# Kernel optimization log

Hardware: AMD Instinct MI355X
Metric: run time of the kernel (lower is better)

The kernel has to match this reference:

```python
import jax, jax.numpy as jnp
import numpy as np

B, T, F, U = 64, 256, 64, 512  # batch, bid_sequence, features, lstm units


def setup_inputs() -> dict:
    key = jax.random.key(0)
    ks = jax.random.split(key, 8)
    sc = 0.05
    return {
        "inputs": jax.random.normal(ks[0], (B, T, F), jnp.float32),
        "kernel": jax.random.normal(ks[1], (F, 4 * U), jnp.float32) * sc,      # LSTM input kernel (i,f,c,o)
        "rec_kernel": jax.random.normal(ks[2], (U, 4 * U), jnp.float32) * sc,  # LSTM recurrent kernel
        "bias": jax.random.normal(ks[3], (4 * U,), jnp.float32) * sc,          # LSTM bias
        "att_W": jax.random.normal(ks[4], (T, T), jnp.float32) * sc,           # row t = weights of attention_denses[t] (first t cols used)
        "att_b": jax.random.normal(ks[5], (T,), jnp.float32) * sc,             # bias of attention_denses[t]
        "out_W": jax.random.normal(ks[6], (U,), jnp.float32) * sc,             # final Dense(1) kernel
        "out_b": jax.random.normal(ks[7], (), jnp.float32) * sc,               # final Dense(1) bias
    }


def reference(inputs, kernel, rec_kernel, bias, att_W, att_b, out_W, out_b):
    Bs, Ts, _ = inputs.shape
    Us = rec_kernel.shape[0]

    # ---- LSTM (keras LSTMCell, gate order i,f,c,o; sigmoid/tanh) ----
    xz = jnp.einsum('btf,fg->btg', inputs, kernel) + bias  # precompute input projection

    def step(carry, z):
        h, c = carry
        g = z + h @ rec_kernel
        i, f, gc, o = jnp.split(g, 4, axis=-1)
        c = jax.nn.sigmoid(f) * c + jax.nn.sigmoid(i) * jnp.tanh(gc)
        h = jax.nn.sigmoid(o) * jnp.tanh(c)
        return (h, c), h

    init = (jnp.zeros((Bs, Us), inputs.dtype), jnp.zeros((Bs, Us), inputs.dtype))
    _, hs = jax.lax.scan(step, init, jnp.swapaxes(xz, 0, 1))
    x = jnp.swapaxes(hs, 0, 1)  # (B, T, U)

    # ---- attention_loop ----
    # keras Attention([x[:t], [x[t]]]) softmaxes over a single key -> weights are
    # exactly 1, so attn output is x[t] tiled t times; transpose + Dense_t(1)
    # collapses to sum(att_W[t, :t]) * x[t] + att_b[t]. Step 0 passes x[0] through.
    t_idx = jnp.arange(Ts)
    tri = (t_idx[None, :] < t_idx[:, None]).astype(x.dtype)  # row t: first t cols valid
    coef = jnp.where(t_idx == 0, jnp.asarray(1.0, x.dtype), jnp.sum(att_W * tri, axis=1))
    shift = jnp.where(t_idx == 0, jnp.asarray(0.0, x.dtype), att_b)
    att = x * coef[None, :, None] + shift[None, :, None]  # (B, T, U)

    # ---- final Dense(1) + reshape + sigmoid ----
    return jax.nn.sigmoid(jnp.einsum('btu,u->bt', att, out_W) + out_b)  # (B, T)
```

## Files before the change

kernel.cpp:

```cpp
#include <hip/hip_runtime.h>
#include <hip/hip_bf16.h>
#include <string.h>

#define B_ 64
#define T_ 256
#define F_ 64
#define U_ 512
#define G4_ 2048
#define KTOT 576
#define KSTEPS 18

typedef __attribute__((ext_vector_type(8))) short short8;
typedef __attribute__((ext_vector_type(4))) float v4f;
typedef __attribute__((ext_vector_type(4))) int i4;
typedef unsigned short u16;

__device__ __forceinline__ float bf2f(u16 b) {
    unsigned int x = ((unsigned int)b) << 16;
    float f; memcpy(&f, &x, 4); return f;
}
__device__ __forceinline__ u16 f2bf(float f) {
    __hip_bfloat16 h = __float2bfloat16(f);
    u16 b; memcpy(&b, &h, 2); return b;
}
__device__ __forceinline__ float sigmoidf_(float x) { return 1.f / (1.f + __expf(-x)); }
__device__ __forceinline__ float tanhf_(float x) {
    float xc = fminf(15.f, fmaxf(-15.f, x));
    float e = __expf(2.f * xc);
    return (e - 1.f) / (e + 1.f);
}

__device__ __forceinline__ float ldany(const void* p, size_t i, int fg) {
    return fg ? ((const float*)p)[i] : bf2f(((const u16*)p)[i]);
}

#define WS_FLAG   0
#define WS_XB     64
#define WS_WP     2097216
#define WS_H2     4456512
#define WS_DOT    4718656
#define WS_BIASF  4784192
#define WS_ATTWF  4792384
#define WS_ATTBF  5054528
#define WS_OUTWF  5055552
#define WS_OUTBF  5057600
#define WS_NEED   5057920

__global__ __launch_bounds__(256) void detect(const unsigned int* __restrict__ w,
                                              int* __restrict__ flag) {
    __shared__ int votes;
    if (threadIdx.x == 0) votes = 0;
    __syncthreads();
    unsigned int v = w[threadIdx.x];
    int e = (v >> 7) & 0xFF;
    if (e >= 100 && e <= 135) atomicAdd(&votes, 1);
    __syncthreads();
    if (threadIdx.x == 0) *flag = (votes < 200) ? 1 : 0;
}

__global__ __launch_bounds__(256) void convert(const void* __restrict__ x,
                                               const void* __restrict__ bias,
                                               const void* __restrict__ attW,
                                               const void* __restrict__ attb,
                                               const void* __restrict__ outW,
                                               const void* __restrict__ outb,
                                               const int* __restrict__ flag,
                                               u16* __restrict__ xb,
                                               float* __restrict__ biasf,
                                               float* __restrict__ attWf,
                                               float* __restrict__ attbf,
                                               float* __restrict__ outWf,
                                               float* __restrict__ outbf,
                                               float* __restrict__ dot,
                                               unsigned int* __restrict__ h2z) {
    int fg = *flag;
    size_t i = (size_t)blockIdx.x * 256 + threadIdx.x;
    if (i < 1048576) {
        float v = ldany(x, i, fg);
        int b = (int)(i >> 14), t = (int)((i >> 6) & 255), f = (int)(i & 63);
        xb[((size_t)t * B_ + b) * F_ + f] = f2bf(v);
        return;
    }
    i -= 1048576;
    if (i < 2048)  { biasf[i] = ldany(bias, i, fg); return; }
    i -= 2048;
    if (i < 65536) { attWf[i] = ldany(attW, i, fg); return; }
    i -= 65536;
    if (i < 256)   { attbf[i] = ldany(attb, i, fg); return; }
    i -= 256;
    if (i < 512)   { outWf[i] = ldany(outW, i, fg); return; }
    i -= 512;
    if (i < 1)     { outbf[i] = ldany(outb, i, fg); return; }
    i -= 1;
    if (i < 16384) { dot[i] = 0.f; return; }
    i -= 16384;
    if (i < 32768) { h2z[i] = 0u; return; }
}

__global__ __launch_bounds__(256) void pack_w(const void* __restrict__ kin,
                                              const void* __restrict__ krec,
                                              const int* __restrict__ flag,
                                              u16* __restrict__ Wp) {
    int fg = *flag;
    int gid = blockIdx.x * 256 + threadIdx.x;
    int lane = gid & 63;
    int frag = gid >> 6;
    int nt = frag / KSTEPS;
    int ks = frag - nt * KSTEPS;
    int kbase = ks * 32 + (lane >> 4) * 8;
    int cp = nt * 16 + (lane & 15);
    int u = cp >> 2, gate = cp & 3;
    int C = gate * U_ + u;
    short8 v;
    for (int j = 0; j < 8; j++) {
        int k = kbase + j;
        float w = (k < F_) ? ldany(kin, (size_t)k * G4_ + C, fg)
                           : ldany(krec, (size_t)(k - F_) * G4_ + C, fg);
        v[j] = (short)f2bf(w);
    }
    *reinterpret_cast<short8*>(Wp + (size_t)gid * 8) = v;
}

__global__ __launch_bounds__(512, 2) void lstm_persist(const u16* __restrict__ xb,
                                                       const float* __restrict__ biasf,
                                                       const float* __restrict__ outWf,
                                                       const u16* __restrict__ Wp,
                                                       u16* __restrict__ h2,
                                                       float* __restrict__ dot) {
    __shared__ __align__(16) u16 stage[16 * 520];
    __shared__ __align__(16) float gbuf[16][132];
    __shared__ float dp[32][16];

    int tid = threadIdx.x;
    int bid = blockIdx.x;
    int rg = bid & 3;
    int gu = bid >> 2;
    int w = tid >> 6, l = tid & 63;
    int nt = gu * 8 + w;

    short8 W[KSTEPS];
    #pragma unroll
    for (int ks = 0; ks < KSTEPS; ks++)
        W[ks] = *reinterpret_cast<const short8*>(Wp + ((size_t)(nt * KSTEPS + ks) * 64 + l) * 8);

    int arow = rg * 16 + (l & 15);
    int koff = (l >> 4) * 8;
    int plr = 2 * w + (l >> 5);
    int pcol = (l & 31) * 16;
    int er = tid >> 5;
    int ui = tid & 31;
    int unit = gu * 32 + ui;
    float bia = biasf[0 * U_ + unit], bif = biasf[1 * U_ + unit];
    float big = biasf[2 * U_ + unit], bio = biasf[3 * U_ + unit];
    float wout = outWf[unit];
    float c = 0.f;

    for (int t = 0; t < T_; t++) {
        u16* hcur = h2 + (size_t)(t & 1) * (B_ * U_);
        const u16* hprev = h2 + (size_t)((t + 1) & 1) * (B_ * U_);
        unsigned int wtag = ((unsigned)(t >> 1) & 1u) ^ 1u;
        unsigned int rpat = ((((unsigned)(t - 1) >> 1) & 1u) ^ 1u) * 0x00010001u;

        i4 q0, q1;
        {
            const void* bp = (const void*)(hprev + (size_t)(rg * 16 + plr) * U_ + pcol);
            int spins = 0;
            for (;;) {
                asm volatile(
                    "global_load_dwordx4 %0, %2, off sc0 sc1\n\t"
                    "global_load_dwordx4 %1, %2, off offset:16 sc0 sc1\n\t"
                    "s_waitcnt vmcnt(0)"
                    : "=v"(q0), "=v"(q1) : "v"(bp) : "memory");
                if (t == 0) break;
                unsigned bad = 0;
                bad |= (((unsigned)q0[0]) ^ rpat) & 0x00010001u;
                bad |= (((unsigned)q0[1]) ^ rpat) & 0x00010001u;
                bad |= (((unsigned)q0[2]) ^ rpat) & 0x00010001u;
                bad |= (((unsigned)q0[3]) ^ rpat) & 0x00010001u;
                bad |= (((unsigned)q1[0]) ^ rpat) & 0x00010001u;
                bad |= (((unsigned)q1[1]) ^ rpat) & 0x00010001u;
                bad |= (((unsigned)q1[2]) ^ rpat) & 0x00010001u;
                bad |= (((unsigned)q1[3]) ^ rpat) & 0x00010001u;
                if (__ballot(bad == 0) == ~0ull) break;
                if (++spins > (1 << 14)) break;
                __builtin_amdgcn_s_sleep(2);
            }
        }
        *reinterpret_cast<i4*>(&stage[plr * 520 + pcol])     = q0;
        *reinterpret_cast<i4*>(&stage[plr * 520 + pcol + 8]) = q1;
        __syncthreads();

        const u16* xrow = xb + ((size_t)t * B_ + arow) * F_;
        short8 a0 = *reinterpret_cast<const short8*>(xrow + koff);
        short8 a1 = *reinterpret_cast<const short8*>(xrow + 32 + koff);
        v4f acc0 = {0.f, 0.f, 0.f, 0.f}, acc1 = {0.f, 0.f, 0.f, 0.f};
        acc0 = __builtin_amdgcn_mfma_f32_16x16x32_bf16(a0, W[0], acc0, 0, 0, 0);
        acc1 = __builtin_amdgcn_mfma_f32_16x16x32_bf16(a1, W[1], acc1, 0, 0, 0);
        #pragma unroll
        for (int ks = 2; ks < KSTEPS; ks += 2) {
            short8 ah0 = *reinterpret_cast<const short8*>(
                &stage[(l & 15) * 520 + (ks - 2) * 32 + koff]);
            short8 ah1 = *reinterpret_cast<const short8*>(
                &stage[(l & 15) * 520 + (ks - 1) * 32 + koff]);
            acc0 = __builtin_amdgcn_mfma_f32_16x16x32_bf16(ah0, W[ks],     acc0, 0, 0, 0);
            acc1 = __builtin_amdgcn_mfma_f32_16x16x32_bf16(ah1, W[ks + 1], acc1, 0, 0, 0);
        }
        v4f acc = acc0 + acc1;

        {
            int col0 = 16 * w + (l & 15);
            int rb = (l >> 4) * 4;
            #pragma unroll
            for (int rr = 0; rr < 4; rr++)
                gbuf[rb + rr][col0] = acc[rr];
        }
        __syncthreads();

        {
            const float* gr = &gbuf[er][4 * ui];
            float ig = sigmoidf_(gr[0] + bia);
            float fg = sigmoidf_(gr[1] + bif);
            float gc = tanhf_(gr[2] + big);
            float og = sigmoidf_(gr[3] + bio);
            c = fg * c + ig * gc;
            float h = og * tanhf_(c);

            float hp = __shfl_xor(h, 1, 64);
            if ((ui & 1) == 0) {
                unsigned int pk = (unsigned int)(((unsigned)f2bf(h)  & 0xFFFEu) | wtag)
                                | ((unsigned int)(((unsigned)f2bf(hp) & 0xFFFEu) | wtag) << 16);
                void* sp = (void*)(hcur + (size_t)(rg * 16 + er) * U_ + unit);
                asm volatile("global_store_dword %0, %1, off sc0 sc1"
                             :: "v"(sp), "v"(pk) : "memory");
            }

            float s = h * wout;
            s += __shfl_xor(s, 1, 64);
            s += __shfl_xor(s, 2, 64);
            s += __shfl_xor(s, 4, 64);
            s += __shfl_xor(s, 8, 64);
            s += __shfl_xor(s, 16, 64);
            if (ui == 0) dp[t & 31][er] = s;
        }

        if ((t & 31) == 31) {
            __syncthreads();
            int t0 = t - 31;
            int tt = tid >> 4, row = tid & 15;
            atomicAdd(&dot[(size_t)(rg * 16 + row) * T_ + (t0 + tt)], dp[tt][row]);
        }
    }
}

__global__ __launch_bounds__(256) void finale(const float* __restrict__ attWf,
                                              const float* __restrict__ attbf,
                                              const float* __restrict__ outWf,
                                              const float* __restrict__ outbf,
                                              const float* __restrict__ dot,
                                              const int* __restrict__ flag,
                                              void* __restrict__ out) {
    __shared__ float red[256];
    int t = blockIdx.x, tid = threadIdx.x;
    int fg = *flag;

    float v = (tid < t) ? attWf[(size_t)t * T_ + tid] : 0.f;
    red[tid] = v; __syncthreads();
    for (int s = 128; s > 0; s >>= 1) { if (tid < s) red[tid] += red[tid + s]; __syncthreads(); }
    float coef = (t == 0) ? 1.f : red[0];
    __syncthreads();
    red[tid] = outWf[tid] + outWf[tid + 256]; __syncthreads();
    for (int s = 128; s > 0; s >>= 1) { if (tid < s) red[tid] += red[tid + s]; __syncthreads(); }
    float sumW = red[0];

    float base = ((t == 0) ? 0.f : attbf[t]) * sumW + outbf[0];

    if (tid < B_) {
        float s = sigmoidf_(coef * dot[(size_t)tid * T_ + t] + base);
        size_t idx = (size_t)tid * T_ + t;
        if (fg) ((float*)out)[idx] = s;
        else    ((u16*)out)[idx] = f2bf(s);
    }
}

extern "C" void kernel_launch(void* const* d_in, const int* in_sizes, int n_in,
                              void* d_out, int out_size, void* d_ws, size_t ws_size,
                              hipStream_t stream) {
    const void* x    = d_in[0];
    const void* kin  = d_in[1];
    const void* krec = d_in[2];
    const void* bias = d_in[3];
    const void* attW = d_in[4];
    const void* attb = d_in[5];
    const void* outW = d_in[6];
    const void* outb = d_in[7];

    if (ws_size < (size_t)WS_NEED) return;

    char* ws = (char*)d_ws;
    int*   flag  = (int*)(ws + WS_FLAG);
    u16*   xb    = (u16*)(ws + WS_XB);
    u16*   Wp    = (u16*)(ws + WS_WP);
    u16*   h2    = (u16*)(ws + WS_H2);
    float* dot   = (float*)(ws + WS_DOT);
    float* biasf = (float*)(ws + WS_BIASF);
    float* attWf = (float*)(ws + WS_ATTWF);
    float* attbf = (float*)(ws + WS_ATTBF);
    float* outWf = (float*)(ws + WS_OUTWF);
    float* outbf = (float*)(ws + WS_OUTBF);

    detect<<<1, 256, 0, stream>>>((const unsigned int*)kin, flag);
    convert<<<4556, 256, 0, stream>>>(x, bias, attW, attb, outW, outb, flag,
                                      xb, biasf, attWf, attbf, outWf, outbf, dot,
                                      (unsigned int*)h2);
    pack_w<<<576, 256, 0, stream>>>(kin, krec, flag, Wp);
    lstm_persist<<<64, 512, 0, stream>>>(xb, biasf, outWf, Wp, h2, dot);
    finale<<<256, 256, 0, stream>>>(attWf, attbf, outWf, outbf, dot, flag, d_out);
}
```

Baseline: 686.5 us.

## Compute LSTM gates in-register via shuffles, double-buffer h stage, drop a barrier

The gate activations are now computed straight from the MFMA accumulators by shuffling the four gate columns within each quad, instead of writing them to a shared gbuf and re-reading after a second __syncthreads. The h staging buffer is double-buffered by timestep parity and the per-wave dot partials get their own shared slots, which removes the remaining extra barrier per step. The input-projection MFMAs are also hoisted ahead of the spin-wait on h so they can overlap the wait. In exchange each lane evaluates four rows of gates with redundant transcendental work across the quad, and occupancy hint drops to one block per CU.

```diff
diff --git a/kernel.cpp b/kernel.cpp
--- a/kernel.cpp
+++ b/kernel.cpp
@@ -121,15 +121,14 @@
     *reinterpret_cast<short8*>(Wp + (size_t)gid * 8) = v;
 }
 
-__global__ __launch_bounds__(512, 2) void lstm_persist(const u16* __restrict__ xb,
+__global__ __launch_bounds__(512, 1) void lstm_persist(const u16* __restrict__ xb,
                                                        const float* __restrict__ biasf,
                                                        const float* __restrict__ outWf,
                                                        const u16* __restrict__ Wp,
                                                        u16* __restrict__ h2,
                                                        float* __restrict__ dot) {
-    __shared__ __align__(16) u16 stage[16 * 520];
-    __shared__ __align__(16) float gbuf[16][132];
-    __shared__ float dp[32][16];
+    __shared__ __align__(16) u16 stage[2][16 * 520];
+    __shared__ float dp[8][32][16];
 
     int tid = threadIdx.x;
     int bid = blockIdx.x;
@@ -147,19 +146,28 @@
     int koff = (l >> 4) * 8;
     int plr = 2 * w + (l >> 5);
     int pcol = (l & 31) * 16;
-    int er = tid >> 5;
-    int ui = tid & 31;
-    int unit = gu * 32 + ui;
+    int ul = (l & 15) >> 2;
+    int unit = 4 * nt + ul;
+    int rb = (l >> 4) * 4;
     float bia = biasf[0 * U_ + unit], bif = biasf[1 * U_ + unit];
     float big = biasf[2 * U_ + unit], bio = biasf[3 * U_ + unit];
     float wout = outWf[unit];
-    float c = 0.f;
+    float creg[4] = {0.f, 0.f, 0.f, 0.f};
+    int qb = l & ~3;
 
     for (int t = 0; t < T_; t++) {
         u16* hcur = h2 + (size_t)(t & 1) * (B_ * U_);
         const u16* hprev = h2 + (size_t)((t + 1) & 1) * (B_ * U_);
         unsigned int wtag = ((unsigned)(t >> 1) & 1u) ^ 1u;
         unsigned int rpat = ((((unsigned)(t - 1) >> 1) & 1u) ^ 1u) * 0x00010001u;
+        u16* stg = stage[t & 1];
+
+        const u16* xrow = xb + ((size_t)t * B_ + arow) * F_;
+        short8 a0 = *reinterpret_cast<const short8*>(xrow + koff);
+        short8 a1 = *reinterpret_cast<const short8*>(xrow + 32 + koff);
+        v4f acc0 = {0.f, 0.f, 0.f, 0.f}, acc1 = {0.f, 0.f, 0.f, 0.f};
+        acc0 = __builtin_amdgcn_mfma_f32_16x16x32_bf16(a0, W[0], acc0, 0, 0, 0);
+        acc1 = __builtin_amdgcn_mfma_f32_16x16x32_bf16(a1, W[1], acc1, 0, 0, 0);
 
         i4 q0, q1;
         {
@@ -186,68 +194,66 @@
                 __builtin_amdgcn_s_sleep(2);
             }
         }
-        *reinterpret_cast<i4*>(&stage[plr * 520 + pcol])     = q0;
-        *reinterpret_cast<i4*>(&stage[plr * 520 + pcol + 8]) = q1;
+        *reinterpret_cast<i4*>(&stg[plr * 520 + pcol])     = q0;
+        *reinterpret_cast<i4*>(&stg[plr * 520 + pcol + 8]) = q1;
         __syncthreads();
 
-        const u16* xrow = xb + ((size_t)t * B_ + arow) * F_;
-        short8 a0 = *reinterpret_cast<const short8*>(xrow + koff);
-        short8 a1 = *reinterpret_cast<const short8*>(xrow + 32 + koff);
-        v4f acc0 = {0.f, 0.f, 0.f, 0.f}, acc1 = {0.f, 0.f, 0.f, 0.f};
-        acc0 = __builtin_amdgcn_mfma_f32_16x16x32_bf16(a0, W[0], acc0, 0, 0, 0);
-        acc1 = __builtin_amdgcn_mfma_f32_16x16x32_bf16(a1, W[1], acc1, 0, 0, 0);
         #pragma unroll
         for (int ks = 2; ks < KSTEPS; ks += 2) {
             short8 ah0 = *reinterpret_cast<const short8*>(
-                &stage[(l & 15) * 520 + (ks - 2) * 32 + koff]);
+                &stg[(l & 15) * 520 + (ks - 2) * 32 + koff]);
             short8 ah1 = *reinterpret_cast<const short8*>(
-                &stage[(l & 15) * 520 + (ks - 1) * 32 + koff]);
+                &stg[(l & 15) * 520 + (ks - 1) * 32 + koff]);
             acc0 = __builtin_amdgcn_mfma_f32_16x16x32_bf16(ah0, W[ks],     acc0, 0, 0, 0);
             acc1 = __builtin_amdgcn_mfma_f32_16x16x32_bf16(ah1, W[ks + 1], acc1, 0, 0, 0);
         }
         v4f acc = acc0 + acc1;
 
-        {
-            int col0 = 16 * w + (l & 15);
-            int rb = (l >> 4) * 4;
+        float h_[4];
+        #pragma unroll
+        for (int rr = 0; rr < 4; rr++) {
+            float gi = __shfl(acc[rr], qb + 0, 64);
+            float gf = __shfl(acc[rr], qb + 1, 64);
+            float gg = __shfl(acc[rr], qb + 2, 64);
+            float go = __shfl(acc[rr], qb + 3, 64);
+            float ig = sigmoidf_(gi + bia);
+            float fg = sigmoidf_(gf + bif);
+            float gc = tanhf_(gg + big);
+            float og = sigmoidf_(go + bio);
+            creg[rr] = fg * creg[rr] + ig * gc;
+            h_[rr] = og * tanhf_(creg[rr]);
+        }
+
+        float hp[4];
+        #pragma unroll
+        for (int rr = 0; rr < 4; rr++) hp[rr] = __shfl_xor(h_[rr], 4, 64);
+        if ((l & 7) == 0) {
             #pragma unroll
-            for (int rr = 0; rr < 4; rr++)
-                gbuf[rb + rr][col0] = acc[rr];
-        }
-        __syncthreads();
-
-        {
-            const float* gr = &gbuf[er][4 * ui];
-            float ig = sigmoidf_(gr[0] + bia);
-            float fg = sigmoidf_(gr[1] + bif);
-            float gc = tanhf_(gr[2] + big);
-            float og = sigmoidf_(gr[3] + bio);
-            c = fg * c + ig * gc;
-            float h = og * tanhf_(c);
-
-            float hp = __shfl_xor(h, 1, 64);
-            if ((ui & 1) == 0) {
-                unsigned int pk = (unsigned int)(((unsigned)f2bf(h)  & 0xFFFEu) | wtag)
-                                | ((unsigned int)(((unsigned)f2bf(hp) & 0xFFFEu) | wtag) << 16);
-                void* sp = (void*)(hcur + (size_t)(rg * 16 + er) * U_ + unit);
+            for (int rr = 0; rr < 4; rr++) {
+                unsigned int pk = (unsigned int)(((unsigned)f2bf(h_[rr]) & 0xFFFEu) | wtag)
+                                | ((unsigned int)(((unsigned)f2bf(hp[rr]) & 0xFFFEu) | wtag) << 16);
+                void* sp = (void*)(hcur + (size_t)(rg * 16 + rb + rr) * U_ + unit);
                 asm volatile("global_store_dword %0, %1, off sc0 sc1"
                              :: "v"(sp), "v"(pk) : "memory");
             }
-
-            float s = h * wout;
-            s += __shfl_xor(s, 1, 64);
-            s += __shfl_xor(s, 2, 64);
+        }
+
+        #pragma unroll
+        for (int rr = 0; rr < 4; rr++) {
+            float s = ((l & 3) == 0) ? h_[rr] * wout : 0.f;
             s += __shfl_xor(s, 4, 64);
             s += __shfl_xor(s, 8, 64);
-            s += __shfl_xor(s, 16, 64);
-            if (ui == 0) dp[t & 31][er] = s;
+            if ((l & 15) == 0) dp[w][t & 31][rb + rr] = s;
         }
 
         if ((t & 31) == 31) {
-            __syncthreads();
             int t0 = t - 31;
-            int tt = tid >> 4, row = tid & 15;
-            atomicAdd(&dot[(size_t)(rg * 16 + row) * T_ + (t0 + tt)], dp[tt][row]);
+            #pragma unroll
+            for (int j = 0; j < 8; j++) {
+                int idx = j * 64 + l;
+                int tt = idx >> 4, row = idx & 15;
+                atomicAdd(&dot[(size_t)(rg * 16 + row) * T_ + (t0 + tt)], dp[w][tt][row]);
+            }
         }
     }
 }
```

Result: slower. 1.493 ms (+117.4%).
